# Performance work log

Hardware: AMD Instinct MI355X
Metric: run time of the kernel (lower is better)

The kernel has to match this reference:

```python
import jax, jax.numpy as jnp
import numpy as np

# Fixed by JastrowNet source: ElectronicSchNet(n_interactions=2, kernel_dim=8, embedding_dim=16, version=1)
BATCH = 512
N_UP, N_DOWN = 16, 16
N_ELEC = N_UP + N_DOWN
N_ATOMS = 8
DIST_FEAT = 32
KERNEL = 8
EMBED = 16
N_LAYERS = 2
W_HIDDEN = 16  # log-spaced hidden dim of the w filter MLP: round(sqrt(32*8))
N_CHAN = 3     # same-spin, anti-spin, nuclear filter channels


def ssp(x):
    # shifted softplus used by SchNet
    return jax.nn.softplus(x) - jnp.log(2.0).astype(x.dtype)


def setup_inputs() -> dict:
    key = jax.random.key(0)
    ks = jax.random.split(key, 16)
    s = lambda fan_in: 1.0 / np.sqrt(fan_in)
    inp = {
        # Gaussian-expanded distance features are non-negative
        'edges_elec': jax.random.uniform(ks[0], (BATCH, N_ELEC, N_ELEC, DIST_FEAT), jnp.float32),
        'edges_nuc': jax.random.uniform(ks[1], (BATCH, N_ELEC, N_ATOMS, DIST_FEAT), jnp.float32),
        # electron spin embedding table (up=0, down=1) and nuclear embeddings Y
        'X_emb': jax.random.normal(ks[2], (2, EMBED), jnp.float32),
        'Y': jax.random.normal(ks[3], (N_ATOMS, KERNEL), jnp.float32),
        # per-layer, per-channel w filter MLP (dist_feat -> hidden -> kernel)
        'wW1': jax.random.normal(ks[4], (N_LAYERS, N_CHAN, DIST_FEAT, W_HIDDEN), jnp.float32) * s(DIST_FEAT),
        'wb1': jnp.zeros((N_LAYERS, N_CHAN, W_HIDDEN), jnp.float32),
        'wW2': jax.random.normal(ks[5], (N_LAYERS, N_CHAN, W_HIDDEN, KERNEL), jnp.float32) * s(W_HIDDEN),
        'wb2': jnp.zeros((N_LAYERS, N_CHAN, KERNEL), jnp.float32),
        # per-layer h subnet (embed -> kernel) and g subnet (kernel -> embed)
        'hW': jax.random.normal(ks[6], (N_LAYERS, EMBED, KERNEL), jnp.float32) * s(EMBED),
        'hb': jnp.zeros((N_LAYERS, KERNEL), jnp.float32),
        'gW': jax.random.normal(ks[7], (N_LAYERS, KERNEL, EMBED), jnp.float32) * s(KERNEL),
        'gb': jnp.zeros((N_LAYERS, EMBED), jnp.float32),
        # readout: Linear(16, 1, bias=False)
        'orb_W': jax.random.normal(ks[8], (EMBED,), jnp.float32) * s(EMBED),
    }
    return inp


def reference(edges_elec, edges_nuc, X_emb, Y, wW1, wb1, wW2, wb2, hW, hb, gW, gb, orb_W):
    B = edges_elec.shape[0]
    spins = jnp.concatenate([jnp.zeros(N_UP, jnp.int32), jnp.ones(N_DOWN, jnp.int32)])
    not_self = ~jnp.eye(N_ELEC, dtype=bool)
    same = ((spins[:, None] == spins[None, :]) & not_self)  # [n,n]
    anti = (spins[:, None] != spins[None, :])

    # initial electron embeddings by spin, broadcast over batch
    x = jnp.broadcast_to(X_emb[spins], (B, N_ELEC, EMBED))

    for l in range(N_LAYERS):
        def w_sub(e, c):
            h1 = ssp(e @ wW1[l, c] + wb1[l, c])
            return ssp(h1 @ wW2[l, c] + wb2[l, c])  # [..., KERNEL]

        w_same = w_sub(edges_elec, 0) * same[None, :, :, None]  # [B,n,n,k]
        w_anti = w_sub(edges_elec, 1) * anti[None, :, :, None]
        w_n = w_sub(edges_nuc, 2)                                # [B,n,m,k]

        hx = ssp(x @ hW[l] + hb[l])                              # [B,n,k]
        # continuous-filter message passing: gather neighbor features, multiply by filter, scatter-sum
        z = jnp.einsum('bijk,bjk->bik', w_same + w_anti, hx)
        z = z + jnp.einsum('bimk,mk->bik', w_n, Y)
        # version 1: single g applied to combined message, residual update
        x = x + z @ gW[l] + gb[l]

    # orbital readout Linear(16,1,bias=False).squeeze(-1).sum(-1)
    return (x @ orb_W).sum(axis=-1)  # [B]
```

## Files before the change

### kernel.cpp

```cpp
#include <hip/hip_runtime.h>
#include <hip/hip_bf16.h>
#include <cstddef>


#define NB   512
#define NE   32
#define NA   8
#define NF   32
#define NH   16
#define NK   8
#define NEMB 16

__device__ __forceinline__ float ssp(float v){
    return fmaxf(v, 0.f) + __logf(1.f + __expf(-fabsf(v))) - 0.6931471805599453f;
}

__device__ __forceinline__ void compute_w(const float4 ev[8],
        const float* __restrict__ sW1, const float* __restrict__ sB1,
        const float* __restrict__ sW2, const float* __restrict__ sB2,
        float w[NK])
{
    float h1[NH];
#pragma unroll
    for (int h = 0; h < NH; h++) h1[h] = sB1[h];
#pragma unroll
    for (int q = 0; q < 8; q++){
        float e4[4] = {ev[q].x, ev[q].y, ev[q].z, ev[q].w};
#pragma unroll
        for (int c = 0; c < 4; c++){
            const float ef = e4[c];
            const float4* w4 = (const float4*)(sW1 + (4*q + c)*NH);
#pragma unroll
            for (int t = 0; t < 4; t++){
                float4 wv = w4[t];
                h1[4*t+0] = fmaf(ef, wv.x, h1[4*t+0]);
                h1[4*t+1] = fmaf(ef, wv.y, h1[4*t+1]);
                h1[4*t+2] = fmaf(ef, wv.z, h1[4*t+2]);
                h1[4*t+3] = fmaf(ef, wv.w, h1[4*t+3]);
            }
        }
    }
#pragma unroll
    for (int h = 0; h < NH; h++) h1[h] = ssp(h1[h]);
    float acc[NK];
#pragma unroll
    for (int k = 0; k < NK; k++) acc[k] = sB2[k];
#pragma unroll
    for (int h = 0; h < NH; h++){
        const float hv = h1[h];
        const float4* w4 = (const float4*)(sW2 + h*NK);
#pragma unroll
        for (int t = 0; t < 2; t++){
            float4 wv = w4[t];
            acc[4*t+0] = fmaf(hv, wv.x, acc[4*t+0]);
            acc[4*t+1] = fmaf(hv, wv.y, acc[4*t+1]);
            acc[4*t+2] = fmaf(hv, wv.z, acc[4*t+2]);
            acc[4*t+3] = fmaf(hv, wv.w, acc[4*t+3]);
        }
    }
#pragma unroll
    for (int k = 0; k < NK; k++) w[k] = ssp(acc[k]);
}

extern "C" __global__ void __launch_bounds__(256, 4)
filters_kernel(const float* __restrict__ edges_elec,
               const float* __restrict__ edges_nuc,
               const float* __restrict__ X_emb,
               const float* __restrict__ Yk,
               const float* __restrict__ wW1, const float* __restrict__ wb1,
               const float* __restrict__ wW2, const float* __restrict__ wb2,
               const float* __restrict__ hW,  const float* __restrict__ hb,
               __hip_bfloat16* __restrict__ w2out,
               float* __restrict__ z1p,
               float* __restrict__ zn1, float* __restrict__ zn2)
{
    __shared__ __align__(16) float s_W1[2*NF*NH];
    __shared__ __align__(16) float s_b1[2*NH];
    __shared__ __align__(16) float s_W2[2*NH*NK];
    __shared__ __align__(16) float s_b2[2*NK];
    __shared__ float s_hx1[2*NK];
    __shared__ float s_Y[NA*NK];

    const int bid = blockIdx.x, t = threadIdx.x;
    const int p = bid >> 9, b = bid & 511;
    const bool isNuc = (p == 4);
    const int qi = p >> 1, qj = p & 1;
    const int cc = isNuc ? 2 : ((qi == qj) ? 0 : 1);

    for (int idx = t; idx < 2*NF*NH; idx += 256){
        int l = idx >> 9, r = idx & 511;
        s_W1[idx] = wW1[(l*3 + cc)*NF*NH + r];
    }
    if (t < 2*NH*NK){
        int l = t >> 7, r = t & 127;
        s_W2[t] = wW2[(l*3 + cc)*NH*NK + r];
    }
    if (t < 2*NH){ int l = t >> 4, r = t & 15; s_b1[t] = wb1[(l*3 + cc)*NH + r]; }
    if (t < 2*NK){ int l = t >> 3, r = t & 7;  s_b2[t] = wb2[(l*3 + cc)*NK + r]; }
    if (isNuc){
        if (t < NA*NK) s_Y[t] = Yk[t];
    } else if (t < 2*NK){
        int s = t >> 3, k = t & 7;
        float acc = hb[k];
#pragma unroll
        for (int e = 0; e < NEMB; e++)
            acc = fmaf(X_emb[s*NEMB + e], hW[e*NK + k], acc);
        s_hx1[t] = ssp(acc);
    }
    __syncthreads();

    const float* src;
    if (isNuc) src = edges_nuc + ((size_t)b*NE*NA + t) * NF;
    else {
        int i = qi*16 + (t >> 4), j = qj*16 + (t & 15);
        src = edges_elec + ((size_t)b*NE*NE + i*NE + j) * NF;
    }
    float4 ev[8];
    {
        const float4* p4 = (const float4*)src;
#pragma unroll
        for (int q = 0; q < 8; q++) ev[q] = p4[q];
    }

    {
        float w[NK];
        compute_w(ev, s_W1, s_b1, s_W2, s_b2, w);
        if (isNuc){
            const int m = t & 7, i = t >> 3;
            float pk[NK];
#pragma unroll
            for (int k = 0; k < NK; k++) pk[k] = w[k] * s_Y[m*NK + k];
#pragma unroll
            for (int off = 4; off > 0; off >>= 1)
#pragma unroll
                for (int k = 0; k < NK; k++) pk[k] += __shfl_down(pk[k], off, 8);
            if (m == 0){
#pragma unroll
                for (int k = 0; k < NK; k++) zn1[((size_t)b*NE + i)*NK + k] = pk[k];
            }
        } else {
            const int i16 = t >> 4, j16 = t & 15;
            const float msk = (cc == 0 && i16 == j16) ? 0.f : 1.f;
            float pk[NK];
#pragma unroll
            for (int k = 0; k < NK; k++) pk[k] = w[k] * msk * s_hx1[qj*NK + k];
#pragma unroll
            for (int off = 8; off > 0; off >>= 1)
#pragma unroll
                for (int k = 0; k < NK; k++) pk[k] += __shfl_down(pk[k], off, 16);
            if (j16 == 0){
                const int i = qi*16 + i16;
#pragma unroll
                for (int k = 0; k < NK; k++)
                    z1p[(((size_t)b*2 + qj)*NE + i)*NK + k] = pk[k];
            }
        }
    }
    {
        float w[NK];
        compute_w(ev, s_W1 + NF*NH, s_b1 + NH, s_W2 + NH*NK, s_b2 + NK, w);
        if (isNuc){
            const int m = t & 7, i = t >> 3;
            float pk[NK];
#pragma unroll
            for (int k = 0; k < NK; k++) pk[k] = w[k] * s_Y[m*NK + k];
#pragma unroll
            for (int off = 4; off > 0; off >>= 1)
#pragma unroll
                for (int k = 0; k < NK; k++) pk[k] += __shfl_down(pk[k], off, 8);
            if (m == 0){
#pragma unroll
                for (int k = 0; k < NK; k++) zn2[((size_t)b*NE + i)*NK + k] = pk[k];
            }
        } else {
            const int i16 = t >> 4, j16 = t & 15;
            const float msk = (cc == 0 && i16 == j16) ? 0.f : 1.f;
            const int i = qi*16 + i16, j = qj*16 + j16;
            union { __hip_bfloat16 h[8]; uint4 u; } pack;
#pragma unroll
            for (int k = 0; k < NK; k++) pack.h[k] = __float2bfloat16(w[k] * msk);
            *(uint4*)&w2out[((size_t)b*NE*NE + i*NE + j)*NK] = pack.u;
        }
    }
}

extern "C" __global__ void __launch_bounds__(256, 4)
update_kernel(const float* __restrict__ X_emb,
              const float* __restrict__ hW,  const float* __restrict__ hb,
              const float* __restrict__ gW,  const float* __restrict__ gb,
              const float* __restrict__ orbW,
              const __hip_bfloat16* __restrict__ w2,
              const float* __restrict__ z1p,
              const float* __restrict__ zn1, const float* __restrict__ zn2,
              float* __restrict__ out)
{
    __shared__ float s_x[NE*NEMB];
    __shared__ float s_z[NE*NK];
    __shared__ float s_hx[NE*NK];
    __shared__ float s_gW[2*NK*NEMB];
    __shared__ float s_gb[2*NEMB];
    __shared__ float s_hW1[NEMB*NK];
    __shared__ float s_hb1[NK];
    __shared__ float s_orb[NEMB];
    __shared__ float s_red[4];

    const int b = blockIdx.x, t = threadIdx.x;

    s_gW[t] = gW[t];
    if (t < 2*NEMB)  s_gb[t]  = gb[t];
    if (t < NEMB*NK) s_hW1[t] = hW[NEMB*NK + t];
    if (t < NK)      s_hb1[t] = hb[NK + t];
    if (t < NEMB)    s_orb[t] = orbW[t];
    {
        const int i = t >> 3, k = t & 7;
        s_z[t] = z1p[(((size_t)b*2 + 0)*NE + i)*NK + k]
               + z1p[(((size_t)b*2 + 1)*NE + i)*NK + k]
               + zn1[((size_t)b*NE + i)*NK + k];
    }
    __syncthreads();
#pragma unroll
    for (int q = 0; q < 2; q++){
        const int idx = q*256 + t, i = idx >> 4, e = idx & 15;
        float acc = s_gb[e];
#pragma unroll
        for (int k = 0; k < NK; k++)
            acc = fmaf(s_z[i*NK + k], s_gW[k*NEMB + e], acc);
        s_x[idx] = X_emb[(i >> 4)*NEMB + e] + acc;
    }
    __syncthreads();
    {
        const int i = t >> 3, k = t & 7;
        float acc = s_hb1[k];
#pragma unroll
        for (int e = 0; e < NEMB; e++)
            acc = fmaf(s_x[i*NEMB + e], s_hW1[e*NK + k], acc);
        s_hx[t] = ssp(acc);
    }
    __syncthreads();
    {
        const int i16 = t >> 4, j16 = t & 15;
#pragma unroll
        for (int qh = 0; qh < 2; qh++){
            const int i = qh*16 + i16;
            float zacc[NK];
#pragma unroll
            for (int k = 0; k < NK; k++) zacc[k] = 0.f;
#pragma unroll
            for (int qj = 0; qj < 2; qj++){
                const int j = qj*16 + j16;
                union { uint4 u; __hip_bfloat16 h[8]; } raw;
                raw.u = *(const uint4*)&w2[((size_t)b*NE*NE + i*NE + j)*NK];
                float pk[NK];
#pragma unroll
                for (int k = 0; k < NK; k++)
                    pk[k] = __bfloat162float(raw.h[k]) * s_hx[j*NK + k];
#pragma unroll
                for (int off = 8; off > 0; off >>= 1)
#pragma unroll
                    for (int k = 0; k < NK; k++) pk[k] += __shfl_down(pk[k], off, 16);
#pragma unroll
                for (int k = 0; k < NK; k++) zacc[k] += pk[k];
            }
            if (j16 == 0){
#pragma unroll
                for (int k = 0; k < NK; k++) s_z[i*NK + k] = zacc[k];
            }
        }
    }
    __syncthreads();
    { const int i = t >> 3, k = t & 7; s_z[t] += zn2[((size_t)b*NE + i)*NK + k]; }
    __syncthreads();
#pragma unroll
    for (int q = 0; q < 2; q++){
        const int idx = q*256 + t, i = idx >> 4, e = idx & 15;
        float acc = s_gb[NEMB + e];
#pragma unroll
        for (int k = 0; k < NK; k++)
            acc = fmaf(s_z[i*NK + k], s_gW[NK*NEMB + k*NEMB + e], acc);
        s_x[idx] += acc;
    }
    __syncthreads();
    float part = (s_x[t] + s_x[t + 256]) * s_orb[t & 15];
#pragma unroll
    for (int off = 32; off > 0; off >>= 1) part += __shfl_down(part, off, 64);
    if ((t & 63) == 0) s_red[t >> 6] = part;
    __syncthreads();
    if (t == 0) out[b] = s_red[0] + s_red[1] + s_red[2] + s_red[3];
}

extern "C" void kernel_launch(void* const* d_in, const int* in_sizes, int n_in,
                              void* d_out, int out_size, void* d_ws, size_t ws_size,
                              hipStream_t stream)
{
    const float* edges_elec = (const float*)d_in[0];
    const float* edges_nuc  = (const float*)d_in[1];
    const float* X_emb      = (const float*)d_in[2];
    const float* Yk         = (const float*)d_in[3];
    const float* wW1        = (const float*)d_in[4];
    const float* wb1        = (const float*)d_in[5];
    const float* wW2        = (const float*)d_in[6];
    const float* wb2        = (const float*)d_in[7];
    const float* hW         = (const float*)d_in[8];
    const float* hb         = (const float*)d_in[9];
    const float* gW         = (const float*)d_in[10];
    const float* gb         = (const float*)d_in[11];
    const float* orbW       = (const float*)d_in[12];

    char* ws = (char*)d_ws;
    __hip_bfloat16* w2 = (__hip_bfloat16*)ws;
    float* z1p = (float*)(ws + 8388608);
    float* zn1 = (float*)(ws + 8388608 + 1048576);
    float* zn2 = (float*)(ws + 8388608 + 1048576 + 524288);

    filters_kernel<<<5*NB, 256, 0, stream>>>(
        edges_elec, edges_nuc, X_emb, Yk, wW1, wb1, wW2, wb2, hW, hb,
        w2, z1p, zn1, zn2);
    update_kernel<<<NB, 256, 0, stream>>>(
        X_emb, hW, hb, gW, gb, orbW, w2, z1p, zn1, zn2, (float*)d_out);
}
```

Before: 159.8 us.

## Compute filter MLPs with bf16 MFMA instead of scalar FMAs

Replaces the per-thread scalar FMA implementation of the two-layer filter MLP with 16x16x32 bf16 MFMA instructions. Weights are held in registers as MFMA A-fragments, edge features are converted to bf16 B-fragments, and hidden activations are reshuffled across lanes between the two matmuls. Shared-memory staging and the block barrier are removed, and reductions move to xor shuffles. This targets the FMA-bound filter computation at the cost of bf16 precision on inputs, weights and hidden activations, plus half-wasted MFMA work for the 8-wide output.

```diff
diff --git a/kernel.cpp b/kernel.cpp
--- a/kernel.cpp
+++ b/kernel.cpp
@@ -1,6 +1,7 @@
 #include <hip/hip_runtime.h>
 #include <hip/hip_bf16.h>
 #include <cstddef>
+#include <cstdint>
 
 
 #define NB   512
@@ -11,55 +12,20 @@
 #define NK   8
 #define NEMB 16
 
+typedef __attribute__((ext_vector_type(8))) short short8;
+typedef __attribute__((ext_vector_type(4))) float f32x4;
+
 __device__ __forceinline__ float ssp(float v){
     return fmaxf(v, 0.f) + __logf(1.f + __expf(-fabsf(v))) - 0.6931471805599453f;
 }
 
-__device__ __forceinline__ void compute_w(const float4 ev[8],
-        const float* __restrict__ sW1, const float* __restrict__ sB1,
-        const float* __restrict__ sW2, const float* __restrict__ sB2,
-        float w[NK])
-{
-    float h1[NH];
-#pragma unroll
-    for (int h = 0; h < NH; h++) h1[h] = sB1[h];
-#pragma unroll
-    for (int q = 0; q < 8; q++){
-        float e4[4] = {ev[q].x, ev[q].y, ev[q].z, ev[q].w};
-#pragma unroll
-        for (int c = 0; c < 4; c++){
-            const float ef = e4[c];
-            const float4* w4 = (const float4*)(sW1 + (4*q + c)*NH);
-#pragma unroll
-            for (int t = 0; t < 4; t++){
-                float4 wv = w4[t];
-                h1[4*t+0] = fmaf(ef, wv.x, h1[4*t+0]);
-                h1[4*t+1] = fmaf(ef, wv.y, h1[4*t+1]);
-                h1[4*t+2] = fmaf(ef, wv.z, h1[4*t+2]);
-                h1[4*t+3] = fmaf(ef, wv.w, h1[4*t+3]);
-            }
-        }
-    }
-#pragma unroll
-    for (int h = 0; h < NH; h++) h1[h] = ssp(h1[h]);
-    float acc[NK];
-#pragma unroll
-    for (int k = 0; k < NK; k++) acc[k] = sB2[k];
-#pragma unroll
-    for (int h = 0; h < NH; h++){
-        const float hv = h1[h];
-        const float4* w4 = (const float4*)(sW2 + h*NK);
-#pragma unroll
-        for (int t = 0; t < 2; t++){
-            float4 wv = w4[t];
-            acc[4*t+0] = fmaf(hv, wv.x, acc[4*t+0]);
-            acc[4*t+1] = fmaf(hv, wv.y, acc[4*t+1]);
-            acc[4*t+2] = fmaf(hv, wv.z, acc[4*t+2]);
-            acc[4*t+3] = fmaf(hv, wv.w, acc[4*t+3]);
-        }
-    }
-#pragma unroll
-    for (int k = 0; k < NK; k++) w[k] = ssp(acc[k]);
+__device__ __forceinline__ short f2bf(float x){
+    unsigned b = __float_as_uint(x);
+    b += 0x7fffu + ((b >> 16) & 1u);
+    return (short)(b >> 16);
+}
+__device__ __forceinline__ unsigned packbf2(float lo, float hi){
+    return (unsigned)(unsigned short)f2bf(lo) | ((unsigned)(unsigned short)f2bf(hi) << 16);
 }
 
 extern "C" __global__ void __launch_bounds__(256, 4)
@@ -74,112 +40,151 @@
                float* __restrict__ z1p,
                float* __restrict__ zn1, float* __restrict__ zn2)
 {
-    __shared__ __align__(16) float s_W1[2*NF*NH];
-    __shared__ __align__(16) float s_b1[2*NH];
-    __shared__ __align__(16) float s_W2[2*NH*NK];
-    __shared__ __align__(16) float s_b2[2*NK];
-    __shared__ float s_hx1[2*NK];
-    __shared__ float s_Y[NA*NK];
-
     const int bid = blockIdx.x, t = threadIdx.x;
     const int p = bid >> 9, b = bid & 511;
     const bool isNuc = (p == 4);
     const int qi = p >> 1, qj = p & 1;
     const int cc = isNuc ? 2 : ((qi == qj) ? 0 : 1);
 
-    for (int idx = t; idx < 2*NF*NH; idx += 256){
-        int l = idx >> 9, r = idx & 511;
-        s_W1[idx] = wW1[(l*3 + cc)*NF*NH + r];
-    }
-    if (t < 2*NH*NK){
-        int l = t >> 7, r = t & 127;
-        s_W2[t] = wW2[(l*3 + cc)*NH*NK + r];
-    }
-    if (t < 2*NH){ int l = t >> 4, r = t & 15; s_b1[t] = wb1[(l*3 + cc)*NH + r]; }
-    if (t < 2*NK){ int l = t >> 3, r = t & 7;  s_b2[t] = wb2[(l*3 + cc)*NK + r]; }
-    if (isNuc){
-        if (t < NA*NK) s_Y[t] = Yk[t];
-    } else if (t < 2*NK){
-        int s = t >> 3, k = t & 7;
-        float acc = hb[k];
-#pragma unroll
-        for (int e = 0; e < NEMB; e++)
-            acc = fmaf(X_emb[s*NEMB + e], hW[e*NK + k], acc);
-        s_hx1[t] = ssp(acc);
-    }
-    __syncthreads();
-
-    const float* src;
-    if (isNuc) src = edges_nuc + ((size_t)b*NE*NA + t) * NF;
-    else {
-        int i = qi*16 + (t >> 4), j = qj*16 + (t & 15);
-        src = edges_elec + ((size_t)b*NE*NE + i*NE + j) * NF;
-    }
-    float4 ev[8];
-    {
-        const float4* p4 = (const float4*)src;
-#pragma unroll
-        for (int q = 0; q < 8; q++) ev[q] = p4[q];
-    }
-
-    {
-        float w[NK];
-        compute_w(ev, s_W1, s_b1, s_W2, s_b2, w);
-        if (isNuc){
-            const int m = t & 7, i = t >> 3;
-            float pk[NK];
-#pragma unroll
-            for (int k = 0; k < NK; k++) pk[k] = w[k] * s_Y[m*NK + k];
-#pragma unroll
-            for (int off = 4; off > 0; off >>= 1)
-#pragma unroll
-                for (int k = 0; k < NK; k++) pk[k] += __shfl_down(pk[k], off, 8);
-            if (m == 0){
-#pragma unroll
-                for (int k = 0; k < NK; k++) zn1[((size_t)b*NE + i)*NK + k] = pk[k];
+    const int lane = t & 63;
+    const int r16 = lane & 15, g4 = lane >> 4;
+    const int wq = (t >> 6) * 4;
+
+    short8 a1[2], a2[2];
+    f32x4 c1[2], c2[2];
+#pragma unroll
+    for (int l = 0; l < 2; l++){
+        const float* W1 = wW1 + (size_t)(l*3 + cc)*NF*NH;
+        const float* W2 = wW2 + (size_t)(l*3 + cc)*NH*NK;
+        short8 s, s2;
+#pragma unroll
+        for (int e = 0; e < 8; e++){
+            s[e] = f2bf(W1[(g4*8 + e)*NH + r16]);
+            const int h = g4*8 + e;
+            s2[e] = (h < NH && r16 < NK) ? f2bf(W2[h*NK + r16]) : (short)0;
+        }
+        a1[l] = s;
+        a2[l] = s2;
+        const float* B1 = wb1 + (l*3 + cc)*NH;
+        const float* B2 = wb2 + (l*3 + cc)*NK;
+        f32x4 cb1, cb2;
+#pragma unroll
+        for (int r = 0; r < 4; r++){
+            const int m = g4*4 + r;
+            cb1[r] = B1[m];
+            cb2[r] = (m < NK) ? B2[m] : 0.f;
+        }
+        c1[l] = cb1; c2[l] = cb2;
+    }
+
+    float hx[4] = {0.f,0.f,0.f,0.f};
+    float Yv[4] = {0.f,0.f,0.f,0.f};
+    if (!isNuc){
+#pragma unroll
+        for (int r = 0; r < 4; r++){
+            const int kk = (g4*4 + r) & 7;
+            float acc = hb[kk];
+#pragma unroll
+            for (int e = 0; e < NEMB; e++)
+                acc = fmaf(X_emb[qj*NEMB + e], hW[e*NK + kk], acc);
+            hx[r] = ssp(acc);
+        }
+    } else {
+        const int m = lane & 7;
+#pragma unroll
+        for (int r = 0; r < 4; r++)
+            Yv[r] = Yk[m*NK + ((g4*4 + r) & 7)];
+    }
+
+    float4 rawA[4], rawB[4];
+    if (!isNuc){
+#pragma unroll
+        for (int g = 0; g < 4; g++){
+            const int i = qi*16 + wq + g;
+            const float* src = edges_elec + (((size_t)b*NE + i)*NE + (qj*16 + r16))*NF + g4*8;
+            rawA[g] = ((const float4*)src)[0];
+            rawB[g] = ((const float4*)src)[1];
+        }
+    } else {
+#pragma unroll
+        for (int g = 0; g < 4; g++){
+            const int gp = wq + g;
+            const int i = 2*gp + (r16 >> 3), m = r16 & 7;
+            const float* src = edges_nuc + (((size_t)b*NE + i)*NA + m)*NF + g4*8;
+            rawA[g] = ((const float4*)src)[0];
+            rawB[g] = ((const float4*)src)[1];
+        }
+    }
+    short8 bfr[4];
+#pragma unroll
+    for (int g = 0; g < 4; g++){
+        short8 s;
+        s[0]=f2bf(rawA[g].x); s[1]=f2bf(rawA[g].y); s[2]=f2bf(rawA[g].z); s[3]=f2bf(rawA[g].w);
+        s[4]=f2bf(rawB[g].x); s[5]=f2bf(rawB[g].y); s[6]=f2bf(rawB[g].z); s[7]=f2bf(rawB[g].w);
+        bfr[g] = s;
+    }
+
+    const int s0 = (g4*32 + r16) & 63;
+    const int s1 = (g4*32 + 16 + r16) & 63;
+
+#pragma unroll
+    for (int g = 0; g < 4; g++){
+#pragma unroll
+        for (int l = 0; l < 2; l++){
+            f32x4 d1 = __builtin_amdgcn_mfma_f32_16x16x32_bf16(a1[l], bfr[g], c1[l], 0, 0, 0);
+            const unsigned p0 = packbf2(ssp(d1[0]), ssp(d1[1]));
+            const unsigned p1 = packbf2(ssp(d1[2]), ssp(d1[3]));
+            unsigned q0 = __shfl(p0, s0, 64);
+            unsigned q1 = __shfl(p1, s0, 64);
+            unsigned q2 = __shfl(p0, s1, 64);
+            unsigned q3 = __shfl(p1, s1, 64);
+            if (g4 >= 2){ q0 = 0u; q1 = 0u; q2 = 0u; q3 = 0u; }
+            union { unsigned u[4]; short8 v; } bb;
+            bb.u[0]=q0; bb.u[1]=q1; bb.u[2]=q2; bb.u[3]=q3;
+            f32x4 d2 = __builtin_amdgcn_mfma_f32_16x16x32_bf16(a2[l], bb.v, c2[l], 0, 0, 0);
+            float wk[4];
+#pragma unroll
+            for (int r = 0; r < 4; r++) wk[r] = ssp(d2[r]);
+
+            if (!isNuc){
+                const int i16 = wq + g;
+                if (cc == 0 && r16 == i16){
+#pragma unroll
+                    for (int r = 0; r < 4; r++) wk[r] = 0.f;
+                }
+                if (l == 0){
+#pragma unroll
+                    for (int off = 1; off < 16; off <<= 1)
+#pragma unroll
+                        for (int r = 0; r < 4; r++) wk[r] += __shfl_xor(wk[r], off, 64);
+                    if (r16 == 0 && g4 < 2){
+                        const int i = qi*16 + i16;
+                        float4 st;
+                        st.x = wk[0]*hx[0]; st.y = wk[1]*hx[1];
+                        st.z = wk[2]*hx[2]; st.w = wk[3]*hx[3];
+                        *(float4*)&z1p[(((size_t)b*2 + qj)*NE + i)*NK + g4*4] = st;
+                    }
+                } else if (g4 < 2){
+                    const int i = qi*16 + i16, j = qj*16 + r16;
+                    uint2 uu;
+                    uu.x = packbf2(wk[0], wk[1]);
+                    uu.y = packbf2(wk[2], wk[3]);
+                    *(uint2*)&w2out[(((size_t)b*NE + i)*NE + j)*NK + g4*4] = uu;
+                }
+            } else {
+#pragma unroll
+                for (int r = 0; r < 4; r++) wk[r] *= Yv[r];
+#pragma unroll
+                for (int off = 1; off < 8; off <<= 1)
+#pragma unroll
+                    for (int r = 0; r < 4; r++) wk[r] += __shfl_xor(wk[r], off, 64);
+                if ((r16 & 7) == 0 && g4 < 2){
+                    const int i = 2*(wq + g) + (r16 >> 3);
+                    float* dst = (l == 0) ? zn1 : zn2;
+                    float4 st; st.x = wk[0]; st.y = wk[1]; st.z = wk[2]; st.w = wk[3];
+                    *(float4*)&dst[((size_t)b*NE + i)*NK + g4*4] = st;
+                }
             }
-        } else {
-            const int i16 = t >> 4, j16 = t & 15;
-            const float msk = (cc == 0 && i16 == j16) ? 0.f : 1.f;
-            float pk[NK];
-#pragma unroll
-            for (int k = 0; k < NK; k++) pk[k] = w[k] * msk * s_hx1[qj*NK + k];
-#pragma unroll
-            for (int off = 8; off > 0; off >>= 1)
-#pragma unroll
-                for (int k = 0; k < NK; k++) pk[k] += __shfl_down(pk[k], off, 16);
-            if (j16 == 0){
-                const int i = qi*16 + i16;
-#pragma unroll
-                for (int k = 0; k < NK; k++)
-                    z1p[(((size_t)b*2 + qj)*NE + i)*NK + k] = pk[k];
-            }
-        }
-    }
-    {
-        float w[NK];
-        compute_w(ev, s_W1 + NF*NH, s_b1 + NH, s_W2 + NH*NK, s_b2 + NK, w);
-        if (isNuc){
-            const int m = t & 7, i = t >> 3;
-            float pk[NK];
-#pragma unroll
-            for (int k = 0; k < NK; k++) pk[k] = w[k] * s_Y[m*NK + k];
-#pragma unroll
-            for (int off = 4; off > 0; off >>= 1)
-#pragma unroll
-                for (int k = 0; k < NK; k++) pk[k] += __shfl_down(pk[k], off, 8);
-            if (m == 0){
-#pragma unroll
-                for (int k = 0; k < NK; k++) zn2[((size_t)b*NE + i)*NK + k] = pk[k];
-            }
-        } else {
-            const int i16 = t >> 4, j16 = t & 15;
-            const float msk = (cc == 0 && i16 == j16) ? 0.f : 1.f;
-            const int i = qi*16 + i16, j = qj*16 + j16;
-            union { __hip_bfloat16 h[8]; uint4 u; } pack;
-#pragma unroll
-            for (int k = 0; k < NK; k++) pack.h[k] = __float2bfloat16(w[k] * msk);
-            *(uint4*)&w2out[((size_t)b*NE*NE + i*NE + j)*NK] = pack.u;
         }
     }
 }
```

Result: faster. 156.5 us (-2.1%).
